# Kernel optimization log

Hardware: AMD Instinct MI355X
Metric: run time of the kernel (lower is better)

The kernel has to match this reference:

```python
import jax, jax.numpy as jnp
import numpy as np

D_MODEL = 512
D_FF = 512
N_EXPERTS = 16
TOP_K = 3
BATCH, SEQ = 1, 2048


def setup_inputs() -> dict:
    key = jax.random.key(0)
    ks = jax.random.split(key, 6)
    x = jax.random.normal(ks[0], (BATCH, SEQ, D_MODEL), dtype=jnp.float32)
    # router gate (std=0.01 per _init_weights)
    gate_w = 0.01 * jax.random.normal(ks[1], (N_EXPERTS, D_MODEL), dtype=jnp.float32)
    expert_bias = jnp.zeros((N_EXPERTS,), dtype=jnp.float32)  # registered buffer, zeros
    # shared SwiGLU expert (std=0.02)
    shared_gate_up = 0.02 * jax.random.normal(ks[2], (2 * D_FF, D_MODEL), dtype=jnp.float32)
    shared_down = 0.02 * jax.random.normal(ks[3], (D_MODEL, D_FF), dtype=jnp.float32)
    # batched routed experts (std=0.02)
    expert_gate_up = 0.02 * jax.random.normal(ks[4], (N_EXPERTS, 2 * D_FF, D_MODEL), dtype=jnp.float32)
    expert_down = 0.02 * jax.random.normal(ks[5], (N_EXPERTS, D_MODEL, D_FF), dtype=jnp.float32)
    return {
        "x": x,
        "gate_w": gate_w,
        "expert_bias": expert_bias,
        "shared_gate_up": shared_gate_up,
        "shared_down": shared_down,
        "expert_gate_up": expert_gate_up,
        "expert_down": expert_down,
    }


def _swiglu(combined):
    gate, up = jnp.split(combined, 2, axis=-1)
    return jax.nn.silu(gate) * up


def reference(x, gate_w, expert_bias, shared_gate_up, shared_down, expert_gate_up, expert_down):
    B, S, D = x.shape
    xf = x.reshape(-1, D)  # [T, D]

    # ---- shared expert (always active) ----
    shared_out = _swiglu(xf @ shared_gate_up.T) @ shared_down.T  # [T, D]

    # ---- router: sigmoid affinity + bias-adjusted top-k ----
    logits = xf @ gate_w.T  # [T, E]
    affinity = jax.nn.sigmoid(logits)
    routing_scores = affinity + expert_bias  # expert_bias buffer (zeros)
    _, sel = jax.lax.top_k(routing_scores, TOP_K)  # [T, K]
    sel_aff = jnp.take_along_axis(affinity, sel, axis=1)  # [T, K]
    gating = sel_aff / (sel_aff.sum(axis=-1, keepdims=True) + 1e-9)  # [T, K]

    # ---- routed experts: per-token SwiGLU with the token's expert weights ----
    # Computed densely per expert then gathered; identical math to the
    # per-token weight-gather in BatchedExperts.
    combined = jnp.einsum('td,efd->tef', xf, expert_gate_up)  # [T, E, 2F]
    hidden = _swiglu(combined)  # [T, E, F]
    expert_out = jnp.einsum('tef,edf->ted', hidden, expert_down)  # [T, E, D]
    sel_out = jnp.take_along_axis(expert_out, sel[:, :, None], axis=1)  # [T, K, D]
    routed_out = jnp.einsum('tk,tkd->td', gating, sel_out)  # [T, D]

    out = shared_out + routed_out  # dropout p=0.0 -> identity
    return out.reshape(B, S, D)
```

## Files before the change

### kernel.cpp

```cpp
#include <hip/hip_runtime.h>

#define T_TOK 2048
#define DM    512
#define DFF   512
#define NE    16

typedef __attribute__((ext_vector_type(8))) short bf16x8;
typedef __attribute__((ext_vector_type(4))) float f32x4;
typedef __attribute__((ext_vector_type(8))) unsigned short us8;

__device__ __forceinline__ unsigned short f2bf(float f) {
  unsigned int u = __float_as_uint(f);
  u += 0x7fffu + ((u >> 16) & 1u);
  return (unsigned short)(u >> 16);
}

__device__ __forceinline__ void dma16(const unsigned short* g, unsigned short* l) {
  __builtin_amdgcn_global_load_lds(
      (const __attribute__((address_space(1))) unsigned int*)g,
      (__attribute__((address_space(3))) unsigned int*)l, 16, 0, 0);
}

#define LDSOFF(row, chunk) ((((row) << 7) + ((((chunk) ^ ((row) & 7))) << 4)))

#define MFMA(a,b,c) __builtin_amdgcn_mfma_f32_16x16x32_bf16((a),(b),(c),0,0,0)

__global__ __launch_bounds__(256) void prep_kernel(
    const float* __restrict__ x, const float* __restrict__ gw,
    const float* __restrict__ bias, int* __restrict__ counts,
    int* __restrict__ list, float* __restrict__ wgt,
    const float* __restrict__ sgu, const float* __restrict__ sdn,
    const float* __restrict__ egu, const float* __restrict__ edn,
    unsigned short* __restrict__ xb,   unsigned short* __restrict__ sgub,
    unsigned short* __restrict__ sdnb, unsigned short* __restrict__ egub,
    unsigned short* __restrict__ ednb, float* __restrict__ out)
{
  const int tid = threadIdx.x;
  if (blockIdx.x >= 512) {
    const int cb = blockIdx.x - 512;
    const int ct = cb * 256 + tid;
    const int CT = 7040 * 256;
    const float4 z4 = {0.f, 0.f, 0.f, 0.f};
    for (int i = ct; i < 262144; i += CT) ((float4*)out)[i] = z4;
    int g = ct;
    const float* s; unsigned short* d; int l;
    if      (g <  131072) { s = x;   d = xb;   l = g;           }
    else if (g <  196608) { s = sgu; d = sgub; l = g -  131072; }
    else if (g <  229376) { s = sdn; d = sdnb; l = g -  196608; }
    else if (g < 1277952) { s = egu; d = egub; l = g -  229376; }
    else                  { s = edn; d = ednb; l = g - 1277952; }
    const float* p = s + (size_t)l * 8;
    float4 v0 = *(const float4*)p;
    float4 v1 = *(const float4*)(p + 4);
    us8 o;
    o[0]=f2bf(v0.x); o[1]=f2bf(v0.y); o[2]=f2bf(v0.z); o[3]=f2bf(v0.w);
    o[4]=f2bf(v1.x); o[5]=f2bf(v1.y); o[6]=f2bf(v1.z); o[7]=f2bf(v1.w);
    *(us8*)(d + (size_t)l * 8) = o;
    return;
  }

  __shared__ float lg[4][16];
  __shared__ int bcnt[16], bbase[16];
  __shared__ int sel_s[4][3], pos_s[4][3];
  __shared__ float g_s[4][3];

  const int w = tid >> 6, lane = tid & 63;
  if (tid < 16) bcnt[tid] = 0;
  const int tok = blockIdx.x * 4 + w;
  const int e = lane & 15, part = lane >> 4;

  const float* xr = x + (size_t)tok * DM + part * 128;
  const float* wr = gw + (size_t)e * DM + part * 128;
  float acc = 0.f;
  #pragma unroll 8
  for (int i = 0; i < 128; i += 4) {
    float4 xv = *(const float4*)(xr + i);
    float4 wv = *(const float4*)(wr + i);
    acc += xv.x*wv.x + xv.y*wv.y + xv.z*wv.z + xv.w*wv.w;
  }
  acc += __shfl_xor(acc, 16);
  acc += __shfl_xor(acc, 32);
  if (lane < 16) lg[w][lane] = 1.f / (1.f + __expf(-acc));
  __syncthreads();

  if (tid < 4) {
    float aff[16], sc[16];
    #pragma unroll
    for (int i = 0; i < 16; ++i) { aff[i] = lg[tid][i]; sc[i] = aff[i] + bias[i]; }
    int sel[3]; float sa[3]; float sum = 0.f;
    #pragma unroll
    for (int k = 0; k < 3; ++k) {
      float best = -1e30f; int bi = 0;
      for (int i = 0; i < 16; ++i) {
        bool used = false;
        for (int j = 0; j < k; ++j) used |= (sel[j] == i);
        if (!used && sc[i] > best) { best = sc[i]; bi = i; }
      }
      sel[k] = bi; sa[k] = aff[bi]; sum += aff[bi];
    }
    float inv = 1.f / (sum + 1e-9f);
    #pragma unroll
    for (int k = 0; k < 3; ++k) {
      int p = atomicAdd(&bcnt[sel[k]], 1);
      sel_s[tid][k] = sel[k]; pos_s[tid][k] = p; g_s[tid][k] = sa[k] * inv;
    }
  }
  __syncthreads();
  if (tid < 16) bbase[tid] = atomicAdd(&counts[tid], bcnt[tid]);
  __syncthreads();
  if (tid < 4) {
    #pragma unroll
    for (int k = 0; k < 3; ++k) {
      int E = sel_s[tid][k];
      int p = bbase[E] + pos_s[tid][k];
      list[E * T_TOK + p] = blockIdx.x * 4 + tid;
      wgt [E * T_TOK + p] = g_s[tid][k];
    }
  }
}

__global__ __launch_bounds__(256, 4) void gemm1_fused(
    const unsigned short* __restrict__ X, const unsigned short* __restrict__ Wsh,
    const unsigned short* __restrict__ Wex, unsigned short* __restrict__ Hall,
    const int* __restrict__ counts, const int* __restrict__ list)
{
  __shared__ unsigned short SA[64][64];
  __shared__ unsigned short SG[64][64];
  __shared__ unsigned short SU[64][64];

  const int n0 = blockIdx.x * 64;
  const int mt = blockIdx.y, z = blockIdx.z;
  int cnt, hb; const unsigned short* W;
  if (z == 0) { cnt = T_TOK; hb = 0; W = Wsh; }
  else {
    const int e = z - 1;
    cnt = counts[e];
    if (mt * 64 >= cnt) return;
    hb = T_TOK;
    for (int i = 0; i < e; ++i) hb += counts[i];
    W = Wex + (size_t)e * (2 * DFF * DM);
  }

  const int tid = threadIdx.x, w = tid >> 6, lane = tid & 63;
  const int r0 = w * 16 + (lane >> 3);
  const int cch = (lane & 7) ^ (r0 & 7);
  const unsigned short* ga[2];
  #pragma unroll
  for (int q = 0; q < 2; ++q) {
    int ra = mt * 64 + r0 + q * 8;
    int rc = ra < cnt ? ra : cnt - 1;
    int tokr = (z == 0) ? rc : list[(z - 1) * T_TOK + rc];
    ga[q] = X + (size_t)tokr * DM + cch * 8;
  }
  const unsigned short *gg[2], *gu[2];
  #pragma unroll
  for (int q = 0; q < 2; ++q) {
    int rb = n0 + r0 + q * 8;
    gg[q] = W + (size_t)rb * DM + cch * 8;
    gu[q] = W + (size_t)(DFF + rb) * DM + cch * 8;
  }
  unsigned short* const lA0 = &SA[w * 16][0];
  unsigned short* const lA1 = &SA[w * 16 + 8][0];
  unsigned short* const lG0 = &SG[w * 16][0];
  unsigned short* const lG1 = &SG[w * 16 + 8][0];
  unsigned short* const lU0 = &SU[w * 16][0];
  unsigned short* const lU1 = &SU[w * 16 + 8][0];

  const int wm = ((tid >> 6) & 1) * 32;
  const int wn = ((tid >> 7) & 1) * 32;
  const int lr = lane & 15, qd = lane >> 4;
  const char* const sa = (const char*)SA;
  const char* const sg = (const char*)SG;
  const char* const su = (const char*)SU;

  const f32x4 z4 = {0.f, 0.f, 0.f, 0.f};
  f32x4 accg[2][2], accu[2][2];
  #pragma unroll
  for (int i = 0; i < 2; ++i)
    #pragma unroll
    for (int j = 0; j < 2; ++j) { accg[i][j] = z4; accu[i][j] = z4; }

  for (int k0 = 0; k0 < DM; k0 += 64) {
    __syncthreads();
    dma16(ga[0] + k0, lA0); dma16(ga[1] + k0, lA1);
    dma16(gg[0] + k0, lG0); dma16(gg[1] + k0, lG1);
    dma16(gu[0] + k0, lU0); dma16(gu[1] + k0, lU1);
    __syncthreads();
    #pragma unroll
    for (int ks = 0; ks < 2; ++ks) {
      const int ch = ks * 4 + qd;
      bf16x8 a0 = *(const bf16x8*)(sa + LDSOFF(wm      + lr, ch));
      bf16x8 a1 = *(const bf16x8*)(sa + LDSOFF(wm + 16 + lr, ch));
      bf16x8 g0 = *(const bf16x8*)(sg + LDSOFF(wn      + lr, ch));
      bf16x8 g1 = *(const bf16x8*)(sg + LDSOFF(wn + 16 + lr, ch));
      bf16x8 u0 = *(const bf16x8*)(su + LDSOFF(wn      + lr, ch));
      bf16x8 u1 = *(const bf16x8*)(su + LDSOFF(wn + 16 + lr, ch));
      accg[0][0] = MFMA(a0, g0, accg[0][0]);
      accg[0][1] = MFMA(a0, g1, accg[0][1]);
      accg[1][0] = MFMA(a1, g0, accg[1][0]);
      accg[1][1] = MFMA(a1, g1, accg[1][1]);
      accu[0][0] = MFMA(a0, u0, accu[0][0]);
      accu[0][1] = MFMA(a0, u1, accu[0][1]);
      accu[1][0] = MFMA(a1, u0, accu[1][0]);
      accu[1][1] = MFMA(a1, u1, accu[1][1]);
    }
  }

  #pragma unroll
  for (int sm = 0; sm < 2; ++sm)
    #pragma unroll
    for (int sn = 0; sn < 2; ++sn) {
      const int col = n0 + wn + sn * 16 + lr;
      #pragma unroll
      for (int r = 0; r < 4; ++r) {
        const int ent = mt * 64 + wm + sm * 16 + qd * 4 + r;
        if (ent < cnt) {
          float g = accg[sm][sn][r];
          float u = accu[sm][sn][r];
          float h = (g / (1.f + __expf(-g))) * u;
          Hall[(size_t)(hb + ent) * DFF + col] = f2bf(h);
        }
      }
    }
}

__global__ __launch_bounds__(256, 4) void gemm2_fused(
    const unsigned short* __restrict__ Hall, const unsigned short* __restrict__ Wsh,
    const unsigned short* __restrict__ Wex, float* __restrict__ out,
    const int* __restrict__ counts, const int* __restrict__ list,
    const float* __restrict__ wgt)
{
  __shared__ unsigned short SA[64][64];
  __shared__ unsigned short SB[64][64];

  const int n0 = blockIdx.x * 64;
  const int mt = blockIdx.y, z = blockIdx.z;
  int cnt, hb; const unsigned short* W;
  if (z == 0) { cnt = T_TOK; hb = 0; W = Wsh; }
  else {
    const int e = z - 1;
    cnt = counts[e];
    if (mt * 64 >= cnt) return;
    hb = T_TOK;
    for (int i = 0; i < e; ++i) hb += counts[i];
    W = Wex + (size_t)e * (DM * DFF);
  }

  const int tid = threadIdx.x, w = tid >> 6, lane = tid & 63;
  const int r0 = w * 16 + (lane >> 3);
  const int cch = (lane & 7) ^ (r0 & 7);
  const unsigned short* ga[2];
  #pragma unroll
  for (int q = 0; q < 2; ++q) {
    int ra = mt * 64 + r0 + q * 8;
    int rc = ra < cnt ? ra : cnt - 1;
    ga[q] = Hall + (size_t)(hb + rc) * DFF + cch * 8;
  }
  const unsigned short* gb[2];
  #pragma unroll
  for (int q = 0; q < 2; ++q)
    gb[q] = W + (size_t)(n0 + r0 + q * 8) * DFF + cch * 8;
  unsigned short* const lA0 = &SA[w * 16][0];
  unsigned short* const lA1 = &SA[w * 16 + 8][0];
  unsigned short* const lB0 = &SB[w * 16][0];
  unsigned short* const lB1 = &SB[w * 16 + 8][0];

  const int wm = ((tid >> 6) & 1) * 32;
  const int wn = ((tid >> 7) & 1) * 32;
  const int lr = lane & 15, qd = lane >> 4;
  const char* const sa = (const char*)SA;
  const char* const sb = (const char*)SB;

  const f32x4 z4 = {0.f, 0.f, 0.f, 0.f};
  f32x4 acc[2][2];
  #pragma unroll
  for (int i = 0; i < 2; ++i)
    #pragma unroll
    for (int j = 0; j < 2; ++j) acc[i][j] = z4;

  for (int k0 = 0; k0 < DFF; k0 += 64) {
    __syncthreads();
    dma16(ga[0] + k0, lA0); dma16(ga[1] + k0, lA1);
    dma16(gb[0] + k0, lB0); dma16(gb[1] + k0, lB1);
    __syncthreads();
    #pragma unroll
    for (int ks = 0; ks < 2; ++ks) {
      const int ch = ks * 4 + qd;
      bf16x8 a0 = *(const bf16x8*)(sa + LDSOFF(wm      + lr, ch));
      bf16x8 a1 = *(const bf16x8*)(sa + LDSOFF(wm + 16 + lr, ch));
      bf16x8 b0 = *(const bf16x8*)(sb + LDSOFF(wn      + lr, ch));
      bf16x8 b1 = *(const bf16x8*)(sb + LDSOFF(wn + 16 + lr, ch));
      acc[0][0] = MFMA(a0, b0, acc[0][0]);
      acc[0][1] = MFMA(a0, b1, acc[0][1]);
      acc[1][0] = MFMA(a1, b0, acc[1][0]);
      acc[1][1] = MFMA(a1, b1, acc[1][1]);
    }
  }

  #pragma unroll
  for (int sm = 0; sm < 2; ++sm)
    #pragma unroll
    for (int sn = 0; sn < 2; ++sn) {
      const int col = n0 + wn + sn * 16 + lr;
      #pragma unroll
      for (int r = 0; r < 4; ++r) {
        const int ent = mt * 64 + wm + sm * 16 + qd * 4 + r;
        if (ent < cnt) {
          float v = acc[sm][sn][r];
          if (z == 0) {
            atomicAdd(out + (size_t)ent * DM + col, v);
          } else {
            const int   tok = list[(z - 1) * T_TOK + ent];
            const float g   = wgt [(z - 1) * T_TOK + ent];
            atomicAdd(out + (size_t)tok * DM + col, g * v);
          }
        }
      }
    }
}

extern "C" void kernel_launch(void* const* d_in, const int* in_sizes, int n_in,
                              void* d_out, int out_size, void* d_ws, size_t ws_size,
                              hipStream_t stream) {
  const float* x    = (const float*)d_in[0];
  const float* gw   = (const float*)d_in[1];
  const float* bias = (const float*)d_in[2];
  const float* sgu  = (const float*)d_in[3];
  const float* sdn  = (const float*)d_in[4];
  const float* egu  = (const float*)d_in[5];
  const float* edn  = (const float*)d_in[6];
  float* out = (float*)d_out;

  char* ws = (char*)d_ws;
  int*            counts = (int*)(ws + 0);
  int*            list   = (int*)(ws + 64);
  float*          wgt    = (float*)(ws + 131136);
  unsigned short* Hall   = (unsigned short*)(ws + 262208);
  unsigned short* xb     = (unsigned short*)(ws + 8650816);
  unsigned short* sgub   = (unsigned short*)(ws + 10747968);
  unsigned short* sdnb   = (unsigned short*)(ws + 11796544);
  unsigned short* egub   = (unsigned short*)(ws + 12320832);
  unsigned short* ednb   = (unsigned short*)(ws + 29098048);
  const size_t need = 37486656;
  if (ws_size < need) return;

  hipMemsetAsync(counts, 0, 64, stream);
  prep_kernel<<<512 + 7040, 256, 0, stream>>>(
      x, gw, bias, counts, list, wgt, sgu, sdn, egu, edn,
      xb, sgub, sdnb, egub, ednb, out);
  gemm1_fused<<<dim3(8, 32, NE + 1), 256, 0, stream>>>(xb, sgub, egub, Hall, counts, list);
  gemm2_fused<<<dim3(8, 32, NE + 1), 256, 0, stream>>>(Hall, sdnb, ednb, out, counts, list, wgt);
}
```

Baseline: 169.0 us.

## Double-buffer LDS tiles in both expert GEMMs to overlap loads with MFMA

Both GEMM kernels now keep two LDS buffers per operand. Each loop step issues the async global-to-LDS copy for the next K-tile before computing on the current one, and one barrier per step replaces the two used before. This is meant to hide global load latency behind MFMA work. It doubles LDS per block (48KB for gemm1), so gemm1's launch bound drops to 3 blocks per CU, which may cost occupancy.

```diff
diff --git a/kernel.cpp b/kernel.cpp
--- a/kernel.cpp
+++ b/kernel.cpp
@@ -119,14 +119,14 @@
   }
 }
 
-__global__ __launch_bounds__(256, 4) void gemm1_fused(
+__global__ __launch_bounds__(256, 3) void gemm1_fused(
     const unsigned short* __restrict__ X, const unsigned short* __restrict__ Wsh,
     const unsigned short* __restrict__ Wex, unsigned short* __restrict__ Hall,
     const int* __restrict__ counts, const int* __restrict__ list)
 {
-  __shared__ unsigned short SA[64][64];
-  __shared__ unsigned short SG[64][64];
-  __shared__ unsigned short SU[64][64];
+  __shared__ unsigned short SA[2][64][64];
+  __shared__ unsigned short SG[2][64][64];
+  __shared__ unsigned short SU[2][64][64];
 
   const int n0 = blockIdx.x * 64;
   const int mt = blockIdx.y, z = blockIdx.z;
@@ -159,12 +159,15 @@
     gg[q] = W + (size_t)rb * DM + cch * 8;
     gu[q] = W + (size_t)(DFF + rb) * DM + cch * 8;
   }
-  unsigned short* const lA0 = &SA[w * 16][0];
-  unsigned short* const lA1 = &SA[w * 16 + 8][0];
-  unsigned short* const lG0 = &SG[w * 16][0];
-  unsigned short* const lG1 = &SG[w * 16 + 8][0];
-  unsigned short* const lU0 = &SU[w * 16][0];
-  unsigned short* const lU1 = &SU[w * 16 + 8][0];
+  unsigned short* lA[2][2]; unsigned short* lG[2][2]; unsigned short* lU[2][2];
+  #pragma unroll
+  for (int b = 0; b < 2; ++b)
+    #pragma unroll
+    for (int q = 0; q < 2; ++q) {
+      lA[b][q] = &SA[b][w * 16 + q * 8][0];
+      lG[b][q] = &SG[b][w * 16 + q * 8][0];
+      lU[b][q] = &SU[b][w * 16 + q * 8][0];
+    }
 
   const int wm = ((tid >> 6) & 1) * 32;
   const int wn = ((tid >> 7) & 1) * 32;
@@ -180,21 +183,34 @@
     #pragma unroll
     for (int j = 0; j < 2; ++j) { accg[i][j] = z4; accu[i][j] = z4; }
 
-  for (int k0 = 0; k0 < DM; k0 += 64) {
+  #pragma unroll
+  for (int q = 0; q < 2; ++q) {
+    dma16(ga[q], lA[0][q]); dma16(gg[q], lG[0][q]); dma16(gu[q], lU[0][q]);
+  }
+
+  #pragma unroll
+  for (int i = 0; i < DM / 64; ++i) {
+    const int b = i & 1;
     __syncthreads();
-    dma16(ga[0] + k0, lA0); dma16(ga[1] + k0, lA1);
-    dma16(gg[0] + k0, lG0); dma16(gg[1] + k0, lG1);
-    dma16(gu[0] + k0, lU0); dma16(gu[1] + k0, lU1);
-    __syncthreads();
+    if (i + 1 < DM / 64) {
+      const int k1 = (i + 1) * 64, nb = b ^ 1;
+      #pragma unroll
+      for (int q = 0; q < 2; ++q) {
+        dma16(ga[q] + k1, lA[nb][q]);
+        dma16(gg[q] + k1, lG[nb][q]);
+        dma16(gu[q] + k1, lU[nb][q]);
+      }
+    }
+    const int bo = b * 8192;
     #pragma unroll
     for (int ks = 0; ks < 2; ++ks) {
       const int ch = ks * 4 + qd;
-      bf16x8 a0 = *(const bf16x8*)(sa + LDSOFF(wm      + lr, ch));
-      bf16x8 a1 = *(const bf16x8*)(sa + LDSOFF(wm + 16 + lr, ch));
-      bf16x8 g0 = *(const bf16x8*)(sg + LDSOFF(wn      + lr, ch));
-      bf16x8 g1 = *(const bf16x8*)(sg + LDSOFF(wn + 16 + lr, ch));
-      bf16x8 u0 = *(const bf16x8*)(su + LDSOFF(wn      + lr, ch));
-      bf16x8 u1 = *(const bf16x8*)(su + LDSOFF(wn + 16 + lr, ch));
+      bf16x8 a0 = *(const bf16x8*)(sa + bo + LDSOFF(wm      + lr, ch));
+      bf16x8 a1 = *(const bf16x8*)(sa + bo + LDSOFF(wm + 16 + lr, ch));
+      bf16x8 g0 = *(const bf16x8*)(sg + bo + LDSOFF(wn      + lr, ch));
+      bf16x8 g1 = *(const bf16x8*)(sg + bo + LDSOFF(wn + 16 + lr, ch));
+      bf16x8 u0 = *(const bf16x8*)(su + bo + LDSOFF(wn      + lr, ch));
+      bf16x8 u1 = *(const bf16x8*)(su + bo + LDSOFF(wn + 16 + lr, ch));
       accg[0][0] = MFMA(a0, g0, accg[0][0]);
       accg[0][1] = MFMA(a0, g1, accg[0][1]);
       accg[1][0] = MFMA(a1, g0, accg[1][0]);
@@ -230,8 +246,8 @@
     const int* __restrict__ counts, const int* __restrict__ list,
     const float* __restrict__ wgt)
 {
-  __shared__ unsigned short SA[64][64];
-  __shared__ unsigned short SB[64][64];
+  __shared__ unsigned short SA[2][64][64];
+  __shared__ unsigned short SB[2][64][64];
 
   const int n0 = blockIdx.x * 64;
   const int mt = blockIdx.y, z = blockIdx.z;
@@ -260,10 +276,14 @@
   #pragma unroll
   for (int q = 0; q < 2; ++q)
     gb[q] = W + (size_t)(n0 + r0 + q * 8) * DFF + cch * 8;
-  unsigned short* const lA0 = &SA[w * 16][0];
-  unsigned short* const lA1 = &SA[w * 16 + 8][0];
-  unsigned short* const lB0 = &SB[w * 16][0];
-  unsigned short* const lB1 = &SB[w * 16 + 8][0];
+  unsigned short* lA[2][2]; unsigned short* lB[2][2];
+  #pragma unroll
+  for (int b = 0; b < 2; ++b)
+    #pragma unroll
+    for (int q = 0; q < 2; ++q) {
+      lA[b][q] = &SA[b][w * 16 + q * 8][0];
+      lB[b][q] = &SB[b][w * 16 + q * 8][0];
+    }
 
   const int wm = ((tid >> 6) & 1) * 32;
   const int wn = ((tid >> 7) & 1) * 32;
@@ -278,18 +298,29 @@
     #pragma unroll
     for (int j = 0; j < 2; ++j) acc[i][j] = z4;
 
-  for (int k0 = 0; k0 < DFF; k0 += 64) {
+  #pragma unroll
+  for (int q = 0; q < 2; ++q) { dma16(ga[q], lA[0][q]); dma16(gb[q], lB[0][q]); }
+
+  #pragma unroll
+  for (int i = 0; i < DFF / 64; ++i) {
+    const int b = i & 1;
     __syncthreads();
-    dma16(ga[0] + k0, lA0); dma16(ga[1] + k0, lA1);
-    dma16(gb[0] + k0, lB0); dma16(gb[1] + k0, lB1);
-    __syncthreads();
+    if (i + 1 < DFF / 64) {
+      const int k1 = (i + 1) * 64, nb = b ^ 1;
+      #pragma unroll
+      for (int q = 0; q < 2; ++q) {
+        dma16(ga[q] + k1, lA[nb][q]);
+        dma16(gb[q] + k1, lB[nb][q]);
+      }
+    }
+    const int bo = b * 8192;
     #pragma unroll
     for (int ks = 0; ks < 2; ++ks) {
       const int ch = ks * 4 + qd;
-      bf16x8 a0 = *(const bf16x8*)(sa + LDSOFF(wm      + lr, ch));
-      bf16x8 a1 = *(const bf16x8*)(sa + LDSOFF(wm + 16 + lr, ch));
-      bf16x8 b0 = *(const bf16x8*)(sb + LDSOFF(wn      + lr, ch));
-      bf16x8 b1 = *(const bf16x8*)(sb + LDSOFF(wn + 16 + lr, ch));
+      bf16x8 a0 = *(const bf16x8*)(sa + bo + LDSOFF(wm      + lr, ch));
+      bf16x8 a1 = *(const bf16x8*)(sa + bo + LDSOFF(wm + 16 + lr, ch));
+      bf16x8 b0 = *(const bf16x8*)(sb + bo + LDSOFF(wn      + lr, ch));
+      bf16x8 b1 = *(const bf16x8*)(sb + bo + LDSOFF(wn + 16 + lr, ch));
       acc[0][0] = MFMA(a0, b0, acc[0][0]);
       acc[0][1] = MFMA(a0, b1, acc[0][1]);
       acc[1][0] = MFMA(a1, b0, acc[1][0]);
```

New measurement: 168.5 us. No clear change (-0.3%).
